# Performance work log

Measured on AMD Instinct MI355X. Metric: run time of the kernel, lower is better.

The kernel has to match this reference:

```python
import jax, jax.numpy as jnp
import numpy as np

NEG_SLOPE = 0.2
EPS = 1e-16  # PyG softmax denominator epsilon


def add_self_loops(edge_index, num_nodes):
    loop = jnp.arange(num_nodes, dtype=edge_index.dtype)
    src = jnp.concatenate([edge_index[0], loop])
    dst = jnp.concatenate([edge_index[1], loop])
    return src, dst


def gat_conv(x, src, dst, W, att_src, att_dst, bias, num_nodes):
    H, C = att_src.shape
    h = (x @ W).reshape(num_nodes, H, C)            # [N,H,C]
    a_s = jnp.einsum('nhc,hc->nh', h, att_src)      # [N,H]
    a_d = jnp.einsum('nhc,hc->nh', h, att_dst)
    e = jax.nn.leaky_relu(a_s[src] + a_d[dst], NEG_SLOPE)  # [E,H]
    m = jax.ops.segment_max(e, dst, num_segments=num_nodes)
    e = jnp.exp(e - m[dst])
    s = jax.ops.segment_sum(e, dst, num_segments=num_nodes)
    alpha = e / (s[dst] + EPS)                      # [E,H]
    out = jax.ops.segment_sum(h[src] * alpha[:, :, None], dst,
                              num_segments=num_nodes)  # [N,H,C]
    return out.reshape(num_nodes, H * C) + bias


def setup_inputs() -> dict:
    key = jax.random.key(0)
    ks = jax.random.split(key, 10)
    N, E, F, Ch = 50000, 800000, 128, 64
    sc = lambda f: 1.0 / np.sqrt(f)
    return {
        'x': jax.random.normal(ks[0], (N, F), jnp.float32),
        'edge_index': jax.random.randint(ks[1], (2, E), 0, N, jnp.int64),
        'W1': jax.random.normal(ks[2], (F, 4 * Ch), jnp.float32) * sc(F),
        'att_src1': jax.random.normal(ks[3], (4, Ch), jnp.float32) * sc(Ch),
        'att_dst1': jax.random.normal(ks[4], (4, Ch), jnp.float32) * sc(Ch),
        'b1': jnp.zeros((4 * Ch,), jnp.float32),
        'W2': jax.random.normal(ks[5], (4 * Ch, Ch), jnp.float32) * sc(4 * Ch),
        'att_src2': jax.random.normal(ks[6], (1, Ch), jnp.float32) * sc(Ch),
        'att_dst2': jax.random.normal(ks[7], (1, Ch), jnp.float32) * sc(Ch),
        'b2': jnp.zeros((Ch,), jnp.float32),
    }


def reference(x, edge_index, W1, att_src1, att_dst1, b1, W2, att_src2, att_dst2, b2):
    N = x.shape[0]
    src, dst = add_self_loops(edge_index, N)
    # dropout layers are inference no-ops
    h = gat_conv(x, src, dst, W1, att_src1, att_dst1, b1, N)
    h = jax.nn.elu(h)
    out = gat_conv(h, src, dst, W2, att_src2, att_dst2, b2, N)
    return out
```

## Files before the change

### kernel.cpp

```cpp
#include <hip/hip_runtime.h>
#include <hip/hip_bf16.h>
#include <stdint.h>


typedef __attribute__((ext_vector_type(8))) short bf16x8;
typedef __attribute__((ext_vector_type(4))) float f32x4;

__device__ __forceinline__ float bf2f(__hip_bfloat16 v) { return __bfloat162float(v); }
__device__ __forceinline__ float bfbits2f(unsigned short s) {
  union { uint32_t u; float f; } v; v.u = ((uint32_t)s) << 16; return v.f;
}
__device__ __forceinline__ unsigned short f2bfbits(float f) {
  union { float f; uint32_t u; } v; v.f = f;
  uint32_t u = v.u;
  return (unsigned short)((u + 0x7fffu + ((u >> 16) & 1u)) >> 16);
}

template <bool BF>
__device__ __forceinline__ float loadF(const void* p, size_t i) {
  if (BF) return bf2f(((const __hip_bfloat16*)p)[i]);
  return ((const float*)p)[i];
}
template <bool I64>
__device__ __forceinline__ int loadI(const void* p, size_t i) {
  if (I64) return (int)((const long long*)p)[i];
  return ((const int*)p)[i];
}
__device__ __forceinline__ float lrelu(float v) { return fmaxf(v, 0.2f * v); }

__global__ __launch_bounds__(256) void detect_zero(
    const uint32_t* __restrict__ xbits, const uint32_t* __restrict__ eibits,
    int* __restrict__ flags, int* __restrict__ zero_region, int nzero) {
  if (blockIdx.x == 0) {
    if (threadIdx.x < 64) {
      const int l = threadIdx.x;
      uint32_t u = xbits[l];
      uint32_t e = (u >> 23) & 0xffu;
      bool plausible = (e < 160u && e > 90u) || (u & 0x7fffffffu) == 0u;
      unsigned long long m1 = __ballot(plausible);
      bool z = (eibits[2 * l + 1] == 0u);
      unsigned long long m2 = __ballot(z);
      if (l == 0) {
        flags[0] = (__popcll(m1) < 32) ? 1 : 0;
        flags[1] = (m2 == ~0ULL) ? 1 : 0;
      }
    }
    return;
  }
  int i = (blockIdx.x - 1) * 256 + threadIdx.x;
  if (i < nzero) zero_region[i] = 0;
}

__global__ __launch_bounds__(256) void hist_prep(
    const void* __restrict__ ei, int E, int* __restrict__ deg,
    int* __restrict__ ppos,
    const void* __restrict__ x, unsigned short* __restrict__ xb, size_t nx,
    const void* __restrict__ W1, unsigned short* __restrict__ w1t, int K1, int N1,
    const void* __restrict__ W2, unsigned short* __restrict__ w2t, int K2, int N2,
    int eb, int nb_cast, int nb_t1, const int* __restrict__ flags) {
  const int b = blockIdx.x;
  const bool f = flags[0] != 0;
  if (b < eb) {
    int e = b * 256 + threadIdx.x;
    if (e >= E) return;
    int d = flags[1] ? loadI<true>(ei, (size_t)E + e) : loadI<false>(ei, (size_t)E + e);
    ppos[e] = atomicAdd(&deg[d], 1);
  } else if (b < eb + nb_cast) {
    if (f) return;
    size_t i = ((size_t)(b - eb) * 256 + threadIdx.x) * 4;
    if (i >= nx) return;
    float4 v = *(const float4*)((const float*)x + i);
    ushort4 o;
    o.x = f2bfbits(v.x); o.y = f2bfbits(v.y);
    o.z = f2bfbits(v.z); o.w = f2bfbits(v.w);
    *(ushort4*)(xb + i) = o;
  } else if (b < eb + nb_cast + nb_t1) {
    int idx = (b - eb - nb_cast) * 256 + threadIdx.x;
    if (idx >= K1 * N1) return;
    int k = idx / N1, n = idx - k * N1;
    float v = f ? loadF<true>(W1, idx) : loadF<false>(W1, idx);
    w1t[(size_t)n * K1 + k] = f2bfbits(v);
  } else {
    int idx = (b - eb - nb_cast - nb_t1) * 256 + threadIdx.x;
    if (idx >= K2 * N2) return;
    int k = idx / N2, n = idx - k * N2;
    float v = f ? loadF<true>(W2, idx) : loadF<false>(W2, idx);
    w2t[(size_t)n * K2 + k] = f2bfbits(v);
  }
}

__global__ __launch_bounds__(256) void scan_onepass(
    const int* __restrict__ deg, int* __restrict__ row_start,
    int* __restrict__ total, int n) {
  __shared__ int buf[256];
  __shared__ int sbase;
  const int t = threadIdx.x;
  const int i = blockIdx.x * 256 + t;
  int v = (i < n) ? deg[i] : 0;
  buf[t] = v;
  __syncthreads();
  for (int o = 1; o < 256; o <<= 1) {
    int x = (t >= o) ? buf[t - o] : 0;
    __syncthreads();
    buf[t] += x;
    __syncthreads();
  }
  if (t == 255) sbase = atomicAdd(total, buf[255]);
  __syncthreads();
  if (i < n) row_start[i] = sbase + buf[t] - v;
}

template <int KC, int NT, int HB>
__device__ __forceinline__ void gemm_body(
    int bx, int by, int tid,
    const unsigned short* __restrict__ A,
    const unsigned short* __restrict__ BT,
    unsigned short* __restrict__ C,
    const void* __restrict__ att_s, const void* __restrict__ att_d,
    float* __restrict__ as_o, float* __restrict__ ad_o,
    float* __restrict__ wself_o,
    int M, int Htot, bool f) {
  const int lane = tid & 63;
  const int col = lane & 15;
  const int quad = lane >> 4;
  const int m0 = bx * 64 + (tid >> 6) * 16;
  const int n0 = by * (NT * 16);
  const int NCOL = Htot * 64;

  int gm = m0 + col;
  if (gm > M - 1) gm = M - 1;
  const unsigned short* arow = A + (size_t)gm * KC + quad * 8;
  const unsigned short* bbase = BT + (size_t)(n0 + col) * KC + quad * 8;

  f32x4 acc[NT] = {};
#pragma unroll
  for (int k0 = 0; k0 < KC; k0 += 32) {
    bf16x8 a = *(const bf16x8*)(arow + k0);
#pragma unroll
    for (int s = 0; s < NT; s++) {
      bf16x8 b = *(const bf16x8*)(bbase + (size_t)s * 16 * KC + k0);
      acc[s] = __builtin_amdgcn_mfma_f32_16x16x32_bf16(a, b, acc[s], 0, 0, 0);
    }
  }
#pragma unroll
  for (int s = 0; s < NT; s++)
#pragma unroll
    for (int r = 0; r < 4; r++) {
      int m = m0 + quad * 4 + r;
      if (m < M) C[(size_t)m * NCOL + n0 + s * 16 + col] = f2bfbits(acc[s][r]);
    }
  const int SC = NT / HB;
#pragma unroll
  for (int h = 0; h < HB; h++) {
    const int gh = by * HB + h;
    float ps[4] = {0.f, 0.f, 0.f, 0.f};
    float pd[4] = {0.f, 0.f, 0.f, 0.f};
#pragma unroll
    for (int j = 0; j < SC; j++) {
      int s = h * SC + j;
      int ci = gh * 64 + j * 16 + col;
      float av = f ? loadF<true>(att_s, ci) : loadF<false>(att_s, ci);
      float dv = f ? loadF<true>(att_d, ci) : loadF<false>(att_d, ci);
#pragma unroll
      for (int r = 0; r < 4; r++) {
        ps[r] += acc[s][r] * av;
        pd[r] += acc[s][r] * dv;
      }
    }
#pragma unroll
    for (int o = 1; o < 16; o <<= 1) {
#pragma unroll
      for (int r = 0; r < 4; r++) {
        ps[r] += __shfl_xor(ps[r], o);
        pd[r] += __shfl_xor(pd[r], o);
      }
    }
    if (col == 0) {
#pragma unroll
      for (int r = 0; r < 4; r++) {
        int m = m0 + quad * 4 + r;
        if (m < M) {
          as_o[m * Htot + gh] = ps[r];
          ad_o[m * Htot + gh] = pd[r];
          wself_o[m * Htot + gh] = __expf(lrelu(ps[r] + pd[r]));
        }
      }
    }
  }
}

__global__ __launch_bounds__(256, 4) void scatter_gemm1(
    const void* __restrict__ ei, int E, const int* __restrict__ row_start,
    const int* __restrict__ ppos, int* __restrict__ col_src,
    int eb, int gb,
    const unsigned short* __restrict__ xb, const void* __restrict__ x,
    const unsigned short* __restrict__ w1t,
    unsigned short* __restrict__ C,
    const void* __restrict__ att_s, const void* __restrict__ att_d,
    float* __restrict__ as_o, float* __restrict__ ad_o,
    float* __restrict__ wself_o,
    int M, int Htot, const int* __restrict__ flags) {
  const int b = blockIdx.x;
  if (b < eb) {
    int e = b * 256 + threadIdx.x;
    if (e >= E) return;
    int s, d;
    if (flags[1]) { s = loadI<true>(ei, e);  d = loadI<true>(ei, (size_t)E + e); }
    else          { s = loadI<false>(ei, e); d = loadI<false>(ei, (size_t)E + e); }
    col_src[row_start[d] + ppos[e]] = s;
  } else {
    const int bb = b - eb;
    const int bx = bb % gb, by = bb / gb;
    const bool f = flags[0] != 0;
    const unsigned short* Ap = f ? (const unsigned short*)x : xb;
    gemm_body<128, 8, 2>(bx, by, threadIdx.x, Ap, w1t, C, att_s, att_d,
                         as_o, ad_o, wself_o, M, Htot, f);
  }
}

template <int KC, int NT, int HB>
__global__ __launch_bounds__(256, 4) void gemm_kernel(
    const unsigned short* __restrict__ A, const unsigned short* __restrict__ BT,
    unsigned short* __restrict__ C,
    const void* __restrict__ att_s, const void* __restrict__ att_d,
    float* __restrict__ as_o, float* __restrict__ ad_o,
    float* __restrict__ wself_o,
    int M, int Htot, const int* __restrict__ flags) {
  gemm_body<KC, NT, HB>(blockIdx.x, blockIdx.y, threadIdx.x, A, BT, C,
                        att_s, att_d, as_o, ad_o, wself_o, M, Htot,
                        flags[0] != 0);
}

__global__ __launch_bounds__(256) void aggregate4(
    const unsigned short* __restrict__ h_in,
    const float* __restrict__ wselfA,
    const float* __restrict__ as_,
    const float* __restrict__ ad_,
    const int* __restrict__ row_start, const int* __restrict__ deg,
    const int* __restrict__ col_src,
    const void* __restrict__ bias,
    unsigned short* __restrict__ out,
    int N, const int* __restrict__ flags) {
  const int dst = blockIdx.x * 4 + (threadIdx.x >> 6);
  if (dst >= N) return;
  const int l = threadIdx.x & 63;
  const int h = l >> 4;
  const int rs = row_start[dst];
  const int dg = deg[dst];
  const float ws = wselfA[dst * 4 + h];
  const float adv = ad_[dst * 4 + h];

  float a0, a1, a2, a3;
  {
    ushort4 sv = *(const ushort4*)(h_in + (size_t)dst * 256 + 4 * l);
    a0 = ws * bfbits2f(sv.x);
    a1 = ws * bfbits2f(sv.y);
    a2 = ws * bfbits2f(sv.z);
    a3 = ws * bfbits2f(sv.w);
  }
  float p = 0.f;
#pragma unroll 4
  for (int i = 0; i < dg; i++) {
    int sn = col_src[rs + i];
    float w = __expf(lrelu(as_[(size_t)sn * 4 + h] + adv));
    p += w;
    ushort4 sv = *(const ushort4*)(h_in + (size_t)sn * 256 + 4 * l);
    a0 += w * bfbits2f(sv.x);
    a1 += w * bfbits2f(sv.y);
    a2 += w * bfbits2f(sv.z);
    a3 += w * bfbits2f(sv.w);
  }
  const float inv = 1.0f / (p + ws + 1e-16f);
  const bool f = flags[0] != 0;
  float b0, b1, b2, b3;
  if (f) {
    b0 = loadF<true>(bias, 4 * l + 0); b1 = loadF<true>(bias, 4 * l + 1);
    b2 = loadF<true>(bias, 4 * l + 2); b3 = loadF<true>(bias, 4 * l + 3);
  } else {
    b0 = loadF<false>(bias, 4 * l + 0); b1 = loadF<false>(bias, 4 * l + 1);
    b2 = loadF<false>(bias, 4 * l + 2); b3 = loadF<false>(bias, 4 * l + 3);
  }
  float o0 = a0 * inv + b0, o1 = a1 * inv + b1;
  float o2 = a2 * inv + b2, o3 = a3 * inv + b3;
  o0 = o0 > 0.f ? o0 : __expf(o0) - 1.f;
  o1 = o1 > 0.f ? o1 : __expf(o1) - 1.f;
  o2 = o2 > 0.f ? o2 : __expf(o2) - 1.f;
  o3 = o3 > 0.f ? o3 : __expf(o3) - 1.f;
  ushort4 ov;
  ov.x = f2bfbits(o0); ov.y = f2bfbits(o1); ov.z = f2bfbits(o2); ov.w = f2bfbits(o3);
  *(ushort4*)(out + (size_t)dst * 256 + 4 * l) = ov;
}

__global__ __launch_bounds__(256) void aggregate1(
    const unsigned short* __restrict__ h_in,
    const float* __restrict__ wselfA,
    const float* __restrict__ as_,
    const float* __restrict__ ad_,
    const int* __restrict__ row_start, const int* __restrict__ deg,
    const int* __restrict__ col_src,
    const void* __restrict__ bias,
    void* __restrict__ out, int N, const int* __restrict__ flags) {
  const int dst = blockIdx.x * 4 + (threadIdx.x >> 6);
  if (dst >= N) return;
  const int l = threadIdx.x & 63;
  const int el = l & 15;
  const int slot = l >> 4;
  const int rs = row_start[dst];
  const int dg = deg[dst];
  const float ws = wselfA[dst];
  const float adv = ad_[dst];

  float a0 = 0.f, a1 = 0.f, a2 = 0.f, a3 = 0.f, p = 0.f;
  if (slot == 0) {
    ushort4 sv = *(const ushort4*)(h_in + (size_t)dst * 64 + 4 * el);
    a0 = ws * bfbits2f(sv.x);
    a1 = ws * bfbits2f(sv.y);
    a2 = ws * bfbits2f(sv.z);
    a3 = ws * bfbits2f(sv.w);
  }
#pragma unroll 2
  for (int i = slot; i < dg; i += 4) {
    int sn = col_src[rs + i];
    float w = __expf(lrelu(as_[sn] + adv));
    p += w;
    ushort4 sv = *(const ushort4*)(h_in + (size_t)sn * 64 + 4 * el);
    a0 += w * bfbits2f(sv.x);
    a1 += w * bfbits2f(sv.y);
    a2 += w * bfbits2f(sv.z);
    a3 += w * bfbits2f(sv.w);
  }
  a0 += __shfl_xor(a0, 16); a0 += __shfl_xor(a0, 32);
  a1 += __shfl_xor(a1, 16); a1 += __shfl_xor(a1, 32);
  a2 += __shfl_xor(a2, 16); a2 += __shfl_xor(a2, 32);
  a3 += __shfl_xor(a3, 16); a3 += __shfl_xor(a3, 32);
  p  += __shfl_xor(p, 16);  p  += __shfl_xor(p, 32);

  if (slot == 0) {
    const float inv = 1.0f / (p + ws + 1e-16f);
    const bool f = flags[0] != 0;
    float b0, b1, b2, b3;
    if (f) {
      b0 = loadF<true>(bias, 4 * el + 0); b1 = loadF<true>(bias, 4 * el + 1);
      b2 = loadF<true>(bias, 4 * el + 2); b3 = loadF<true>(bias, 4 * el + 3);
    } else {
      b0 = loadF<false>(bias, 4 * el + 0); b1 = loadF<false>(bias, 4 * el + 1);
      b2 = loadF<false>(bias, 4 * el + 2); b3 = loadF<false>(bias, 4 * el + 3);
    }
    float o0 = a0 * inv + b0, o1 = a1 * inv + b1;
    float o2 = a2 * inv + b2, o3 = a3 * inv + b3;
    size_t ob = (size_t)dst * 64 + 4 * el;
    if (f) {
      ushort4 ov;
      ov.x = f2bfbits(o0); ov.y = f2bfbits(o1);
      ov.z = f2bfbits(o2); ov.w = f2bfbits(o3);
      *(ushort4*)((unsigned short*)out + ob) = ov;
    } else {
      float4 ov; ov.x = o0; ov.y = o1; ov.z = o2; ov.w = o3;
      *(float4*)((float*)out + ob) = ov;
    }
  }
}

extern "C" void kernel_launch(void* const* d_in, const int* in_sizes, int n_in,
                              void* d_out, int out_size, void* d_ws, size_t ws_size,
                              hipStream_t stream) {
  const void* x    = d_in[0];
  const void* ei   = d_in[1];
  const void* W1   = d_in[2];
  const void* as1w = d_in[3];
  const void* ad1w = d_in[4];
  const void* b1   = d_in[5];
  const void* W2   = d_in[6];
  const void* as2w = d_in[7];
  const void* ad2w = d_in[8];
  const void* b2   = d_in[9];

  const int N  = out_size / 64;
  const int F  = in_sizes[0] / N;
  const int E  = in_sizes[1] / 2;
  const int H1 = in_sizes[3] / 64;
  const int D1 = H1 * 64;
  const int D2 = 64;

  size_t off = 0;
  auto alloc = [&](size_t bytes) -> void* {
    void* p = (char*)d_ws + off;
    off += (bytes + 255) & ~(size_t)255;
    return p;
  };
  int* flags = (int*)alloc(2 * sizeof(int));
  __hip_bfloat16* h1 = (__hip_bfloat16*)alloc((size_t)N * D1 * 2);
  __hip_bfloat16* x2 = (__hip_bfloat16*)alloc((size_t)N * D1 * 2);
  __hip_bfloat16* h2 = h1;
  unsigned short* xb  = (unsigned short*)alloc((size_t)N * F * 2);
  unsigned short* w1t = (unsigned short*)alloc((size_t)D1 * F * 2);
  unsigned short* w2t = (unsigned short*)alloc((size_t)D2 * D1 * 2);
  float* as1 = (float*)alloc((size_t)N * H1 * 4);
  float* ad1 = (float*)alloc((size_t)N * H1 * 4);
  float* wself1 = (float*)alloc((size_t)N * H1 * 4);
  float* as2 = (float*)alloc((size_t)N * 4);
  float* ad2 = (float*)alloc((size_t)N * 4);
  float* wself2 = (float*)alloc((size_t)N * 4);
  int* zero_region = (int*)alloc((size_t)(N + 64) * 4);
  int* deg = zero_region;
  int* total = zero_region + N;
  int* row_start = (int*)alloc((size_t)(N + 1) * 4);
  int* col_src = (int*)alloc((size_t)E * 4);
  int* ppos = (int*)alloc((size_t)E * 4);
  (void)ws_size; (void)n_in;

  const int nb = (N + 255) / 256;
  const int eb = (E + 255) / 256;
  const int db = (N + 3) / 4;
  const int gb = (N + 63) / 64;
  const int nzero = N + 64;
  const int zb = (nzero + 255) / 256;

  const size_t nx = (size_t)N * F;
  const int nb_cast = (int)((nx / 4 + 255) / 256);
  const int nb_t1 = (F * D1 + 255) / 256;
  const int nb_t2 = (D1 * D2 + 255) / 256;

  detect_zero<<<1 + zb, 256, 0, stream>>>((const uint32_t*)x, (const uint32_t*)ei,
                                          flags, zero_region, nzero);
  hist_prep<<<eb + nb_cast + nb_t1 + nb_t2, 256, 0, stream>>>(
      ei, E, deg, ppos, x, xb, nx, W1, w1t, F, D1, W2, w2t, D1, D2,
      eb, nb_cast, nb_t1, flags);
  scan_onepass<<<nb, 256, 0, stream>>>(deg, row_start, total, N);
  scatter_gemm1<<<eb + gb * 2, 256, 0, stream>>>(
      ei, E, row_start, ppos, col_src, eb, gb,
      xb, x, w1t, (unsigned short*)h1, as1w, ad1w, as1, ad1, wself1, N, H1, flags);
  aggregate4<<<db, 256, 0, stream>>>((const unsigned short*)h1, wself1, as1, ad1,
                                     row_start, deg, col_src, b1,
                                     (unsigned short*)x2, N, flags);
  gemm_kernel<256, 4, 1><<<dim3(gb, 1), 256, 0, stream>>>(
      (const unsigned short*)x2, w2t, (unsigned short*)h2, as2w, ad2w,
      as2, ad2, wself2, N, 1, flags);
  aggregate1<<<db, 256, 0, stream>>>((const unsigned short*)h2, wself2, as2, ad2,
                                     row_start, deg, col_src, b2, d_out, N, flags);
}
```

Baseline: 293.4 us.

## Fuse layer-2 projection and attention logits into layer-1 aggregation kernel

Layer-1 aggregation now keeps each node's ELU output in LDS and immediately multiplies it by the transposed W2 (one output channel per lane), then writes h2 and computes the layer-2 attention scalars and self-loop weight with a wavefront reduction. This removes the x2 intermediate buffer's write and re-read and one kernel launch (the separate MFMA GEMM). In exchange the second GEMM runs as scalar FMAs on CUDA-core-style ALUs, with each lane streaming a 512-byte W2 row per node, which adds ALU and L1/L2 load pressure to a gather-bound kernel.

```diff
diff --git a/kernel.cpp b/kernel.cpp
--- a/kernel.cpp
+++ b/kernel.cpp
@@ -218,20 +218,7 @@
   }
 }
 
-template <int KC, int NT, int HB>
-__global__ __launch_bounds__(256, 4) void gemm_kernel(
-    const unsigned short* __restrict__ A, const unsigned short* __restrict__ BT,
-    unsigned short* __restrict__ C,
-    const void* __restrict__ att_s, const void* __restrict__ att_d,
-    float* __restrict__ as_o, float* __restrict__ ad_o,
-    float* __restrict__ wself_o,
-    int M, int Htot, const int* __restrict__ flags) {
-  gemm_body<KC, NT, HB>(blockIdx.x, blockIdx.y, threadIdx.x, A, BT, C,
-                        att_s, att_d, as_o, ad_o, wself_o, M, Htot,
-                        flags[0] != 0);
-}
-
-__global__ __launch_bounds__(256) void aggregate4(
+__global__ __launch_bounds__(256) void aggregate4_g2(
     const unsigned short* __restrict__ h_in,
     const float* __restrict__ wselfA,
     const float* __restrict__ as_,
@@ -239,10 +226,16 @@
     const int* __restrict__ row_start, const int* __restrict__ deg,
     const int* __restrict__ col_src,
     const void* __restrict__ bias,
-    unsigned short* __restrict__ out,
+    const unsigned short* __restrict__ w2t,
+    const void* __restrict__ att_s2, const void* __restrict__ att_d2,
+    unsigned short* __restrict__ h2o,
+    float* __restrict__ as2o, float* __restrict__ ad2o,
+    float* __restrict__ wself2o,
     int N, const int* __restrict__ flags) {
+  __shared__ float o_lds[4][256];
   const int dst = blockIdx.x * 4 + (threadIdx.x >> 6);
   if (dst >= N) return;
+  const int wv = threadIdx.x >> 6;
   const int l = threadIdx.x & 63;
   const int h = l >> 4;
   const int rs = row_start[dst];
@@ -288,7 +281,41 @@
   o3 = o3 > 0.f ? o3 : __expf(o3) - 1.f;
   ushort4 ov;
   ov.x = f2bfbits(o0); ov.y = f2bfbits(o1); ov.z = f2bfbits(o2); ov.w = f2bfbits(o3);
-  *(ushort4*)(out + (size_t)dst * 256 + 4 * l) = ov;
+  float4 st;
+  st.x = bfbits2f(ov.x); st.y = bfbits2f(ov.y);
+  st.z = bfbits2f(ov.z); st.w = bfbits2f(ov.w);
+  *(float4*)&o_lds[wv][4 * l] = st;
+
+  const unsigned short* wrow = w2t + (size_t)l * 256;
+  float outn = 0.f;
+#pragma unroll
+  for (int kk = 0; kk < 256; kk += 8) {
+    bf16x8 wvv = *(const bf16x8*)(wrow + kk);
+    const float* ob = &o_lds[wv][kk];
+    outn += ob[0] * bfbits2f((unsigned short)wvv[0]);
+    outn += ob[1] * bfbits2f((unsigned short)wvv[1]);
+    outn += ob[2] * bfbits2f((unsigned short)wvv[2]);
+    outn += ob[3] * bfbits2f((unsigned short)wvv[3]);
+    outn += ob[4] * bfbits2f((unsigned short)wvv[4]);
+    outn += ob[5] * bfbits2f((unsigned short)wvv[5]);
+    outn += ob[6] * bfbits2f((unsigned short)wvv[6]);
+    outn += ob[7] * bfbits2f((unsigned short)wvv[7]);
+  }
+  h2o[(size_t)dst * 64 + l] = f2bfbits(outn);
+
+  float avs = f ? loadF<true>(att_s2, l) : loadF<false>(att_s2, l);
+  float avd = f ? loadF<true>(att_d2, l) : loadF<false>(att_d2, l);
+  float ps2 = outn * avs, pd2 = outn * avd;
+#pragma unroll
+  for (int o = 1; o < 64; o <<= 1) {
+    ps2 += __shfl_xor(ps2, o);
+    pd2 += __shfl_xor(pd2, o);
+  }
+  if (l == 0) {
+    as2o[dst] = ps2;
+    ad2o[dst] = pd2;
+    wself2o[dst] = __expf(lrelu(ps2 + pd2));
+  }
 }
 
 __global__ __launch_bounds__(256) void aggregate1(
@@ -390,8 +417,7 @@
   };
   int* flags = (int*)alloc(2 * sizeof(int));
   __hip_bfloat16* h1 = (__hip_bfloat16*)alloc((size_t)N * D1 * 2);
-  __hip_bfloat16* x2 = (__hip_bfloat16*)alloc((size_t)N * D1 * 2);
-  __hip_bfloat16* h2 = h1;
+  __hip_bfloat16* h2 = (__hip_bfloat16*)alloc((size_t)N * D2 * 2);
   unsigned short* xb  = (unsigned short*)alloc((size_t)N * F * 2);
   unsigned short* w1t = (unsigned short*)alloc((size_t)D1 * F * 2);
   unsigned short* w2t = (unsigned short*)alloc((size_t)D2 * D1 * 2);
@@ -430,12 +456,9 @@
   scatter_gemm1<<<eb + gb * 2, 256, 0, stream>>>(
       ei, E, row_start, ppos, col_src, eb, gb,
       xb, x, w1t, (unsigned short*)h1, as1w, ad1w, as1, ad1, wself1, N, H1, flags);
-  aggregate4<<<db, 256, 0, stream>>>((const unsigned short*)h1, wself1, as1, ad1,
-                                     row_start, deg, col_src, b1,
-                                     (unsigned short*)x2, N, flags);
-  gemm_kernel<256, 4, 1><<<dim3(gb, 1), 256, 0, stream>>>(
-      (const unsigned short*)x2, w2t, (unsigned short*)h2, as2w, ad2w,
-      as2, ad2, wself2, N, 1, flags);
+  aggregate4_g2<<<db, 256, 0, stream>>>(
+      (const unsigned short*)h1, wself1, as1, ad1, row_start, deg, col_src, b1,
+      w2t, as2w, ad2w, (unsigned short*)h2, as2, ad2, wself2, N, flags);
   aggregate1<<<db, 256, 0, stream>>>((const unsigned short*)h2, wself2, as2, ad2,
                                      row_start, deg, col_src, b2, d_out, N, flags);
 }
```

Measured after the change: 442.0 us. +50.6%, slower.
